# Kernel tuning notes

Hardware: AMD Instinct MI355X
Metric: run time of the kernel (lower is better)

The kernel has to match this reference:

```python
import jax, jax.numpy as jnp
import numpy as np

DIM = 512; H = 8; KH = 2; G = 4; DH = 64        # dim, q heads, kv heads, GQA group, head dim
BALL = 128; SEL = 64; TOPK = 2; PDIM = 3        # sliding ball, compress/selection block, topk, pos dim
SCALE = DH ** -0.5


def _rms_norm(x, gamma):
    return x * jax.lax.rsqrt(jnp.mean(x * x, axis=-1, keepdims=True) + 1e-6) * gamma


def _rotary(t):
    # t: (B, h, S, DH); GPT-NeoX style rotate-half rotary embedding
    S = t.shape[-2]
    inv = 1.0 / (10000.0 ** (jnp.arange(0, DH, 2, dtype=jnp.float32) / DH))
    f = jnp.arange(S, dtype=jnp.float32)[:, None] * inv          # (S, DH/2)
    cos = jnp.concatenate([jnp.cos(f), jnp.cos(f)], -1)
    sin = jnp.concatenate([jnp.sin(f), jnp.sin(f)], -1)
    t1, t2 = jnp.split(t, 2, -1)
    return t * cos + jnp.concatenate([-t2, t1], -1) * sin


def _forward(x, pos, pe_w, pe_b, gamma, wq, wk, wv, k_pos, v_pos,
             k_w1, k_b1, k_w2, k_b2, v_w1, v_b1, v_w2, v_b2,
             mem_k, mem_v, w_combine, w_out, num_batches):
    B = num_batches
    # relative position of leaves wrt ball center (no-grad in original)
    p = jax.lax.stop_gradient(pos).reshape(-1, SEL, PDIM)
    rel = (p - p.mean(axis=1, keepdims=True)).reshape(-1, PDIM)
    x = x + rel @ pe_w + pe_b
    x = x.reshape(B, -1, DIM)
    S = x.shape[1]
    nb = S // SEL
    h = _rms_norm(x, gamma)
    q = (h @ wq).reshape(B, S, H, DH).transpose(0, 2, 1, 3)      # (B,H,S,DH)
    k = (h @ wk).reshape(B, S, KH, DH).transpose(0, 2, 1, 3)     # (B,KH,S,DH)
    v = (h @ wv).reshape(B, S, KH, DH).transpose(0, 2, 1, 3)
    qr, kr = _rotary(q), _rotary(k)

    # --- compressed branch: per-block intra-pos emb + MLP compression ---
    kb = k.reshape(B, KH, nb, SEL, DH) + k_pos[None, :, None]
    vb = v.reshape(B, KH, nb, SEL, DH) + v_pos[None, :, None]
    ck = jax.nn.relu(kb.reshape(B, KH, nb, SEL * DH) @ k_w1 + k_b1) @ k_w2 + k_b2
    cv = jax.nn.relu(vb.reshape(B, KH, nb, SEL * DH) @ v_w1 + v_b1) @ v_w2 + v_b2
    ck = jnp.concatenate([jnp.broadcast_to(mem_k[None], (B, KH, 1, DH)), ck], axis=2)
    cv = jnp.concatenate([jnp.broadcast_to(mem_v[None], (B, KH, 1, DH)), cv], axis=2)
    qg = qr.reshape(B, KH, G, S, DH)
    csim = jnp.einsum('bkgsd,bknd->bkgsn', qg, ck) * SCALE
    cattn = jax.nn.softmax(csim, axis=-1)
    cout = jnp.einsum('bkgsn,bknd->bkgsd', cattn, cv).reshape(B, H, S, DH)

    # --- top-k block selection from compressed attention importance ---
    imp = cattn[..., 1:].mean(axis=2)                            # share over grouped q heads: (B,KH,S,nb)
    imp_blk = imp.reshape(B, KH, nb, SEL, nb).mean(axis=3)       # per query block: (B,KH,nb,nb)
    _, sel = jax.lax.top_k(imp_blk, TOPK)                        # (B,KH,nb,TOPK)

    # --- fine branch: each query block attends own + TOPK selected blocks ---
    kblk = kr.reshape(B, KH, nb, SEL, DH)
    vblk = v.reshape(B, KH, nb, SEL, DH)
    gather = jax.vmap(jax.vmap(lambda t, s: t[s]))               # (nb,SEL,DH),(nb,TOPK)->(nb,TOPK,SEL,DH)
    fk = jnp.concatenate([gather(kblk, sel), kblk[:, :, :, None]], axis=3)
    fv = jnp.concatenate([gather(vblk, sel), vblk[:, :, :, None]], axis=3)
    fk = fk.reshape(B, KH, nb, (TOPK + 1) * SEL, DH)
    fv = fv.reshape(B, KH, nb, (TOPK + 1) * SEL, DH)
    qb = qr.reshape(B, KH, G, nb, SEL, DH)
    fsim = jnp.einsum('bkgnqd,bknmd->bkgnqm', qb, fk) * SCALE
    fout = jnp.einsum('bkgnqm,bknmd->bkgnqd', jax.nn.softmax(fsim, -1), fv)
    fout = fout.reshape(B, H, S, DH)

    # --- sliding branch: MiniBallAttn = plain SDPA within balls of size 128 ---
    nw = S // BALL
    qw = qr.reshape(B, H, nw, BALL, DH)
    kw = jnp.repeat(kr, G, axis=1).reshape(B, H, nw, BALL, DH)
    vw = jnp.repeat(v, G, axis=1).reshape(B, H, nw, BALL, DH)
    ssim = jnp.einsum('bhnqd,bhnkd->bhnqk', qw, kw) * SCALE
    sout = jnp.einsum('bhnqk,bhnkd->bhnqd', jax.nn.softmax(ssim, -1), vw)
    sout = sout.reshape(B, H, S, DH)

    # --- sigmoid-gated strategy combine, merge heads, out projection ---
    gates = jax.nn.sigmoid(h @ w_combine).reshape(B, S, H, 3).transpose(0, 2, 1, 3)
    out = gates[..., 0:1] * cout + gates[..., 1:2] * fout + gates[..., 2:3] * sout
    out = out.transpose(0, 2, 1, 3).reshape(B, S, H * DH) @ w_out
    return out.reshape(-1, DIM)


def setup_inputs() -> dict:
    key = jax.random.key(0)
    ks = jax.random.split(key, 16)
    Bn, S = 8, 4096
    N = Bn * S
    CD = SEL * DH
    def lin(k, fi, fo):
        return (jax.random.normal(k, (fi, fo), jnp.float32) / np.sqrt(fi)).astype(jnp.float32)
    return {
        'x': jax.random.normal(ks[0], (N, DIM), jnp.float32),
        'pos': jax.random.normal(ks[1], (N, PDIM), jnp.float32),
        'pe_w': lin(ks[2], PDIM, DIM),
        'pe_b': jnp.zeros((DIM,), jnp.float32),
        'gamma': jnp.ones((DIM,), jnp.float32),
        'wq': lin(ks[3], DIM, H * DH),
        'wk': lin(ks[4], DIM, KH * DH),
        'wv': lin(ks[5], DIM, KH * DH),
        'k_pos': jax.random.normal(ks[6], (KH, SEL, DH), jnp.float32) * 0.02,
        'v_pos': jax.random.normal(ks[7], (KH, SEL, DH), jnp.float32) * 0.02,
        'k_w1': lin(ks[8], CD, CD), 'k_b1': jnp.zeros((CD,), jnp.float32),
        'k_w2': lin(ks[9], CD, DH), 'k_b2': jnp.zeros((DH,), jnp.float32),
        'v_w1': lin(ks[10], CD, CD), 'v_b1': jnp.zeros((CD,), jnp.float32),
        'v_w2': lin(ks[11], CD, DH), 'v_b2': jnp.zeros((DH,), jnp.float32),
        'mem_k': jax.random.normal(ks[12], (KH, 1, DH), jnp.float32) * 0.02,
        'mem_v': jax.random.normal(ks[13], (KH, 1, DH), jnp.float32) * 0.02,
        'w_combine': lin(ks[14], DIM, 3 * H),
        'w_out': lin(ks[15], H * DH, DIM),
        'num_batches': 8,
    }


def reference(x, pos, pe_w, pe_b, gamma, wq, wk, wv, k_pos, v_pos,
              k_w1, k_b1, k_w2, k_b2, v_w1, v_b1, v_w2, v_b2,
              mem_k, mem_v, w_combine, w_out, num_batches):
    return _forward(x, pos, pe_w, pe_b, gamma, wq, wk, wv, k_pos, v_pos,
                    k_w1, k_b1, k_w2, k_b2, v_w1, v_b1, v_w2, v_b2,
                    mem_k, mem_v, w_combine, w_out, num_batches)
```

## Files before the change

### kernel.cpp

```cpp
#include <hip/hip_runtime.h>
#include <stdint.h>

#define DEVI static __device__ __forceinline__
typedef unsigned short u16;
typedef __bf16 bhalf8 __attribute__((ext_vector_type(8)));
typedef float f32x4 __attribute__((ext_vector_type(4)));

DEVI u16 f2bf(float f) {
  union { float f; unsigned u; } v; v.f = f;
  unsigned r = v.u + 0x7FFFu + ((v.u >> 16) & 1u);
  return (u16)(r >> 16);
}
DEVI float bf2f(u16 h) {
  union { unsigned u; float f; } v; v.u = ((unsigned)h) << 16;
  return v.f;
}
DEVI f32x4 MFMA(bhalf8 a, bhalf8 b, f32x4 c) {
  return __builtin_amdgcn_mfma_f32_16x16x32_bf16(a, b, c, 0, 0, 0);
}
DEVI bhalf8 LD8(const u16* p) { return *(const bhalf8*)p; }
DEVI f32x4 zero4() { f32x4 z = {0.f, 0.f, 0.f, 0.f}; return z; }

#define GLDS16(gp, lp) __builtin_amdgcn_global_load_lds( \
    (const __attribute__((address_space(1))) void*)(gp), \
    (__attribute__((address_space(3))) void*)(lp), 16, 0, 0)


__global__ __launch_bounds__(64) void nsa_pos_mean(const float* __restrict__ pos, float* __restrict__ pm) {
  int blk = blockIdx.x, l = threadIdx.x;
  const float* p = pos + (size_t)(blk * 64 + l) * 3;
  float a = p[0], b = p[1], c = p[2];
#pragma unroll
  for (int o = 32; o; o >>= 1) { a += __shfl_down(a, o); b += __shfl_down(b, o); c += __shfl_down(c, o); }
  if (l == 0) { pm[blk*3+0] = a * (1.f/64.f); pm[blk*3+1] = b * (1.f/64.f); pm[blk*3+2] = c * (1.f/64.f); }
}

__global__ __launch_bounds__(256) void nsa_hnorm(const float* __restrict__ x, const float* __restrict__ pos,
    const float* __restrict__ pm, const float* __restrict__ pew, const float* __restrict__ peb,
    const float* __restrict__ gamma, u16* __restrict__ hhi, u16* __restrict__ hlo) {
  int n = blockIdx.x, t = threadIdx.x;
  int blk = n >> 6;
  float r0 = pos[(size_t)n*3+0] - pm[blk*3+0];
  float r1 = pos[(size_t)n*3+1] - pm[blk*3+1];
  float r2 = pos[(size_t)n*3+2] - pm[blk*3+2];
  int c0 = t, c1 = t + 256;
  const float* xr = x + (size_t)n * 512;
  float v0 = xr[c0] + r0*pew[c0] + r1*pew[512+c0] + r2*pew[1024+c0] + peb[c0];
  float v1 = xr[c1] + r0*pew[c1] + r1*pew[512+c1] + r2*pew[1024+c1] + peb[c1];
  float ss = v0*v0 + v1*v1;
#pragma unroll
  for (int o = 32; o; o >>= 1) ss += __shfl_down(ss, o);
  __shared__ float red[4];
  if ((t & 63) == 0) red[t >> 6] = ss;
  __syncthreads();
  float rms = 1.0f / sqrtf((red[0]+red[1]+red[2]+red[3]) * (1.0f/512.0f) + 1e-6f);
  float h0 = v0 * rms * gamma[c0], h1 = v1 * rms * gamma[c1];
  u16 a0 = f2bf(h0); hhi[(size_t)n*512+c0] = a0; hlo[(size_t)n*512+c0] = f2bf(h0 - bf2f(a0));
  u16 a1 = f2bf(h1); hhi[(size_t)n*512+c1] = a1; hlo[(size_t)n*512+c1] = f2bf(h1 - bf2f(a1));
}

__global__ __launch_bounds__(256) void nsa_wcatT(const float* __restrict__ wq, const float* __restrict__ wk,
    const float* __restrict__ wv, const float* __restrict__ wc, u16* __restrict__ hi, u16* __restrict__ lo) {
  int idx = blockIdx.x * 256 + threadIdx.x;
  if (idx >= 896*512) return;
  int k = idx & 511, n = idx >> 9;
  float v;
  if (n < 512) v = wq[(size_t)k*512 + n];
  else if (n < 640) v = wk[(size_t)k*128 + n - 512];
  else if (n < 768) v = wv[(size_t)k*128 + n - 640];
  else if (n < 792) v = wc[(size_t)k*24 + n - 768];
  else v = 0.f;
  u16 h = f2bf(v); hi[idx] = h; lo[idx] = f2bf(v - bf2f(h));
}

__global__ __launch_bounds__(256) void nsa_rope_tab(float* __restrict__ ct, float* __restrict__ st) {
  int idx = blockIdx.x * 256 + threadIdx.x;
  if (idx >= 4096*32) return;
  int s = idx >> 5, i = idx & 31;
  float e = (float)(2*i) * (1.0f/64.0f);
  float inv = 1.0f / powf(10000.0f, e);
  float f = (float)s * inv;
  ct[idx] = cosf(f); st[idx] = sinf(f);
}

__global__ __launch_bounds__(256) void nsa_rope_k(const float* __restrict__ k32, const float* __restrict__ ct,
    const float* __restrict__ st, u16* __restrict__ kb) {
  int idx = blockIdx.x * 256 + threadIdx.x;
  int d = idx & 31, s = (idx >> 5) & 4095, kh = (idx >> 17) & 1, b = idx >> 18;
  const float* kr = k32 + ((size_t)(b*4096 + s))*128 + kh*64;
  float t1 = kr[d], t2 = kr[d+32];
  float c = ct[s*32+d], sn = st[s*32+d];
  size_t ob = (((size_t)(b*2 + kh))*4096 + s)*64;
  kb[ob+d] = f2bf(t1*c - t2*sn);
  kb[ob+d+32] = f2bf(t2*c + t1*sn);
}

__global__ __launch_bounds__(256) void nsa_vT(const float* __restrict__ v32, u16* __restrict__ vT) {
  int blk = blockIdx.x;
  int st = (blk & 63) * 64, kh = (blk >> 6) & 1, b = blk >> 7;
  __shared__ float tile[64][65];
  int t = threadIdx.x;
  int s = t >> 2, c0 = (t & 3) * 16;
  const float* src = v32 + ((size_t)(b*4096 + st + s))*128 + kh*64;
#pragma unroll
  for (int j = 0; j < 16; ++j) tile[s][c0+j] = src[c0+j];
  __syncthreads();
  int d = t >> 2, s0 = (t & 3) * 16;
  u16* dst = vT + (((size_t)(b*2 + kh))*64 + d)*4096 + st + s0;
#pragma unroll
  for (int j = 0; j < 16; ++j) dst[j] = f2bf(tile[s0+j][d]);
}

__global__ __launch_bounds__(256) void nsa_kb(const float* __restrict__ src, const float* __restrict__ pe,
    u16* __restrict__ ohi, u16* __restrict__ olo) {
  int idx = blockIdx.x * 256 + threadIdx.x;
  int c = idx & 4095, m = idx >> 12;
  int sl = c >> 6, d = c & 63;
  int n = m & 63, kh = (m >> 6) & 1, b = m >> 7;
  int s = n*64 + sl;
  float v = src[((size_t)(b*4096 + s))*128 + kh*64 + d] + pe[(kh*64 + sl)*64 + d];
  u16 h = f2bf(v); ohi[idx] = h;
  if (olo) olo[idx] = f2bf(v - bf2f(h));
}

__global__ __launch_bounds__(256) void nsa_wT(const float* __restrict__ src, u16* __restrict__ dhi,
    u16* __restrict__ dlo, int K, int N) {
  __shared__ float tile[64][65];
  int k0 = blockIdx.x * 64, n0 = blockIdx.y * 64;
  int t = threadIdx.x, r = t >> 2, c0 = (t & 3) * 16;
#pragma unroll
  for (int j = 0; j < 16; ++j) tile[r][c0+j] = src[(size_t)(k0+r)*N + n0 + c0 + j];
  __syncthreads();
  size_t ob = (size_t)(n0 + r)*K + k0 + c0;
#pragma unroll
  for (int j = 0; j < 16; ++j) {
    float v = tile[c0+j][r];
    u16 h = f2bf(v); dhi[ob+j] = h;
    if (dlo) dlo[ob+j] = f2bf(v - bf2f(h));
  }
}

__global__ __launch_bounds__(256) void nsa_init_c(const float* __restrict__ mem, const float* __restrict__ b2,
    float* __restrict__ c32) {
  int idx = blockIdx.x * 256 + threadIdx.x;
  if (idx >= 81920) return;
  int d = idx & 63, n = (idx >> 6) % 80, kh = (idx / (80*64)) & 1;
  c32[idx] = (n == 0) ? mem[kh*64 + d] : ((n <= 64) ? b2[d] : 0.f);
}

__global__ __launch_bounds__(256) void nsa_red64(const float* __restrict__ part, float* __restrict__ c32) {
  int idx = blockIdx.x * 256 + threadIdx.x;
  int m = idx >> 6, d = idx & 63;
  float s = 0.f;
#pragma unroll
  for (int kc = 0; kc < 8; ++kc) s += part[((size_t)kc*1024 + m)*64 + d];
  int bkh = m >> 6, n = m & 63;
  c32[(((size_t)bkh)*80 + 1 + n)*64 + d] += s;
}

template<bool SPLIT>
__global__ __launch_bounds__(256) void nsa_mlp_fuse(const float* __restrict__ part,
    const float* __restrict__ bias, u16* __restrict__ oh, u16* __restrict__ ol) {
  size_t i = ((size_t)blockIdx.x * 256 + threadIdx.x) * 4;
  int c = (int)(i & 4095);
  float4 a = *(const float4*)&part[i];
  float4 b = *(const float4*)&part[(size_t)4194304 + i];
  float v0 = fmaxf(a.x + b.x + bias[c+0], 0.f);
  float v1 = fmaxf(a.y + b.y + bias[c+1], 0.f);
  float v2 = fmaxf(a.z + b.z + bias[c+2], 0.f);
  float v3 = fmaxf(a.w + b.w + bias[c+3], 0.f);
  u16 h0 = f2bf(v0), h1 = f2bf(v1), h2 = f2bf(v2), h3 = f2bf(v3);
  ((unsigned long long*)oh)[i >> 2] = (unsigned long long)h0 | ((unsigned long long)h1 << 16) |
                                      ((unsigned long long)h2 << 32) | ((unsigned long long)h3 << 48);
  if (SPLIT) {
    u16 l0 = f2bf(v0 - bf2f(h0)), l1 = f2bf(v1 - bf2f(h1));
    u16 l2 = f2bf(v2 - bf2f(h2)), l3 = f2bf(v3 - bf2f(h3));
    ((unsigned long long*)ol)[i >> 2] = (unsigned long long)l0 | ((unsigned long long)l1 << 16) |
                                        ((unsigned long long)l2 << 32) | ((unsigned long long)l3 << 48);
  }
}

__global__ __launch_bounds__(256) void nsa_ckcv(const float* __restrict__ ck32, const float* __restrict__ cv32,
    u16* __restrict__ ckh, u16* __restrict__ ckl, u16* __restrict__ cvT) {
  int idx = blockIdx.x * 256 + threadIdx.x;
  if (idx < 81920) {
    float v = ck32[idx];
    u16 h = f2bf(v); ckh[idx] = h; ckl[idx] = f2bf(v - bf2f(h));
  } else if (idx < 81920 + 8*2*64*96) {
    int j = idx - 81920;
    int cc = j % 96, d = (j / 96) & 63, bkh = j / (96*64);
    float v = (cc < 80) ? cv32[((size_t)bkh*80 + cc)*64 + d] : 0.f;
    cvT[j] = f2bf(v);
  }
}

__global__ __launch_bounds__(256) void nsa_comb_bf(const float* __restrict__ c, u16* __restrict__ oh) {
  int i = blockIdx.x * 256 + threadIdx.x;
  float4 v = ((const float4*)c)[i];
  u16 h0 = f2bf(v.x), h1 = f2bf(v.y), h2 = f2bf(v.z), h3 = f2bf(v.w);
  ((unsigned long long*)oh)[i] = (unsigned long long)h0 | ((unsigned long long)h1 << 16) |
                                 ((unsigned long long)h2 << 32) | ((unsigned long long)h3 << 48);
}

__global__ __launch_bounds__(256) void nsa_sentinel(float* __restrict__ o, int n, float val) {
  int i = blockIdx.x * 256 + threadIdx.x;
  if (i < n) o[i] = val;
}

template<bool SPLIT, int EPI>
__global__ __launch_bounds__(256) void nsa_gemm(const u16* __restrict__ Ah, const u16* __restrict__ Al,
    const u16* __restrict__ Bh, const u16* __restrict__ Bl, int K, int N,
    const float* __restrict__ p_cos, float* __restrict__ p_sin,
    u16* __restrict__ out_hi, u16* __restrict__ out_lo,
    float* __restrict__ ok, float* __restrict__ ov, float* __restrict__ og) {
  constexpr int NB = SPLIT ? 4 : 2;
  __shared__ u16 sm[NB * 2 * 4096];
  const int t = threadIdx.x, w = t >> 6, l = t & 63;
  const int wm = w >> 1, wn = w & 1;
  const int MBn = gridDim.x;
  const int nwg = MBn * gridDim.y;
  const int bid = blockIdx.y * MBn + blockIdx.x;
  const int swz = (bid & 7) * (nwg >> 3) + (bid >> 3);
  const int m0 = (swz % MBn) * 128, n0 = (swz / MBn) * 128;
  const int klen = K / (int)gridDim.z;
  const int kb0 = blockIdx.z * klen;
  const int row = l & 15;
  const int kc8 = ((l >> 4) ^ ((l >> 1) & 3)) * 8;
  const int gsc = ((l & 3) ^ ((l >> 3) & 3)) * 8;
  const int sr = l >> 2;
  f32x4 acc[4][4];
#pragma unroll
  for (int a = 0; a < 4; ++a)
#pragma unroll
    for (int b = 0; b < 4; ++b) acc[a][b] = zero4();

  auto STAGE = [&](int buf, int k0) {
    u16* base = sm + buf * NB * 4096;
#pragma unroll
    for (int s2 = 0; s2 < 2; ++s2) {
      int seg = w*2 + s2;
      int r = seg*16 + sr;
      size_t ga = (size_t)(m0 + r)*K + k0 + gsc;
      size_t gb = (size_t)(n0 + r)*K + k0 + gsc;
      GLDS16(&Ah[ga], base + seg*512);
      GLDS16(&Bh[gb], base + 4096 + seg*512);
      if (SPLIT) {
        GLDS16(&Al[ga], base + 2*4096 + seg*512);
        GLDS16(&Bl[gb], base + 3*4096 + seg*512);
      }
    }
  };

  const int nt = klen >> 5;
  STAGE(0, kb0);
  __syncthreads();
  int cur = 0;
  for (int kt = 0; kt < nt; ++kt) {
    if (kt + 1 < nt) STAGE(cur ^ 1, kb0 + (kt + 1) * 32);
    u16* bA  = sm + cur * NB * 4096;
    u16* bB  = bA + 4096;
    u16* bAl = bA + 2*4096;
    u16* bBl = bA + 3*4096;
    bhalf8 af[4], afl[4];
#pragma unroll
    for (int mf = 0; mf < 4; ++mf) {
      af[mf] = LD8(&bA[(wm*64 + mf*16 + row)*32 + kc8]);
      if (SPLIT) afl[mf] = LD8(&bAl[(wm*64 + mf*16 + row)*32 + kc8]);
    }
#pragma unroll
    for (int nf = 0; nf < 4; ++nf) {
      bhalf8 bfh = LD8(&bB[(wn*64 + nf*16 + row)*32 + kc8]);
      bhalf8 bfl;
      if (SPLIT) bfl = LD8(&bBl[(wn*64 + nf*16 + row)*32 + kc8]);
#pragma unroll
      for (int mf = 0; mf < 4; ++mf) {
        acc[mf][nf] = MFMA(af[mf], bfh, acc[mf][nf]);
        if (SPLIT) {
          acc[mf][nf] = MFMA(af[mf], bfl, acc[mf][nf]);
          acc[mf][nf] = MFMA(afl[mf], bfh, acc[mf][nf]);
        }
      }
    }
    __syncthreads();
    cur ^= 1;
  }
  if constexpr (EPI == 0) {
    if (n0 < 512) {
#pragma unroll
      for (int mf = 0; mf < 4; ++mf)
#pragma unroll
        for (int i = 0; i < 4; ++i) {
          int r = m0 + wm*64 + mf*16 + (l >> 4)*4 + i;
          int s = r & 4095, b = r >> 12;
#pragma unroll
          for (int nf = 0; nf < 2; ++nf) {
            int c = n0 + wn*64 + nf*16 + (l & 15);
            int hq = c >> 6, dd = c & 31;
            float t1 = acc[mf][nf][i], t2 = acc[mf][nf+2][i];
            float cs = p_cos[s*32 + dd], sn = p_sin[s*32 + dd];
            float o1 = t1*cs - t2*sn, o2 = t2*cs + t1*sn;
            size_t ob = (((size_t)(b*8 + hq))*4096 + s)*64;
            u16 h1 = f2bf(o1); out_hi[ob+dd] = h1;    out_lo[ob+dd] = f2bf(o1 - bf2f(h1));
            u16 h2 = f2bf(o2); out_hi[ob+dd+32] = h2; out_lo[ob+dd+32] = f2bf(o2 - bf2f(h2));
          }
        }
    } else {
#pragma unroll
      for (int mf = 0; mf < 4; ++mf)
#pragma unroll
        for (int nf = 0; nf < 4; ++nf)
#pragma unroll
          for (int i = 0; i < 4; ++i) {
            int r = m0 + wm*64 + mf*16 + (l >> 4)*4 + i;
            int c = n0 + wn*64 + nf*16 + (l & 15);
            float v = acc[mf][nf][i];
            if (n0 == 512) ok[(size_t)r*128 + (c - 512)] = v;
            else if (n0 == 640) ov[(size_t)r*128 + (c - 640)] = v;
            else if (c < 792) og[(size_t)r*24 + (c - 768)] = 1.0f / (1.0f + expf(-v));
          }
    }
  } else if constexpr (EPI == 2) {
#pragma unroll
    for (int mf = 0; mf < 4; ++mf)
#pragma unroll
      for (int nf = 0; nf < 4; ++nf)
#pragma unroll
        for (int i = 0; i < 4; ++i) {
          int r = m0 + wm*64 + mf*16 + (l >> 4)*4 + i;
          int c = n0 + wn*64 + nf*16 + (l & 15);
          p_sin[(size_t)r*N + c] = acc[mf][nf][i];
        }
  } else {
    const int M = MBn * 128;
#pragma unroll
    for (int mf = 0; mf < 4; ++mf)
#pragma unroll
      for (int nf = 0; nf < 4; ++nf)
#pragma unroll
        for (int i = 0; i < 4; ++i) {
          int r = m0 + wm*64 + mf*16 + (l >> 4)*4 + i;
          int c = n0 + wn*64 + nf*16 + (l & 15);
          p_sin[((size_t)blockIdx.z * M + r) * (size_t)N + c] = acc[mf][nf][i];
        }
  }
}

template<bool SPLIT>
__global__ __launch_bounds__(256) void nsa_gemm64(const u16* __restrict__ Ah, const u16* __restrict__ Al,
    const u16* __restrict__ Bh, const u16* __restrict__ Bl, float* __restrict__ part) {
  constexpr int NB = SPLIT ? 4 : 2;
  __shared__ u16 sm[NB * 2 * 2048];
  const int t = threadIdx.x, w = t >> 6, l = t & 63;
  const int mt = blockIdx.x, kc = blockIdx.y;
  const int row = l & 15;
  const int kc8 = ((l >> 4) ^ ((l >> 1) & 3)) * 8;
  const int gsc = ((l & 3) ^ ((l >> 3) & 3)) * 8;
  const int sr = l >> 2;
  f32x4 acc[4];
#pragma unroll
  for (int a = 0; a < 4; ++a) acc[a] = zero4();

  auto STAGE = [&](int buf, int k0) {
    u16* base = sm + buf * NB * 2048;
    int r = w*16 + sr;
    size_t ga = (size_t)(mt*64 + r)*4096 + k0 + gsc;
    size_t gb = (size_t)r*4096 + k0 + gsc;
    GLDS16(&Ah[ga], base + w*512);
    GLDS16(&Bh[gb], base + 2048 + w*512);
    if (SPLIT) {
      GLDS16(&Al[ga], base + 2*2048 + w*512);
      GLDS16(&Bl[gb], base + 3*2048 + w*512);
    }
  };

  STAGE(0, kc*512);
  __syncthreads();
  int cur = 0;
  for (int kt = 0; kt < 16; ++kt) {
    if (kt + 1 < 16) STAGE(cur ^ 1, kc*512 + (kt + 1) * 32);
    u16* bA  = sm + cur * NB * 2048;
    u16* bB  = bA + 2048;
    u16* bAl = bA + 2*2048;
    u16* bBl = bA + 3*2048;
    bhalf8 a = LD8(&bA[(w*16 + row)*32 + kc8]);
    bhalf8 al;
    if (SPLIT) al = LD8(&bAl[(w*16 + row)*32 + kc8]);
#pragma unroll
    for (int nf = 0; nf < 4; ++nf) {
      bhalf8 b = LD8(&bB[(nf*16 + row)*32 + kc8]);
      bhalf8 bl;
      if (SPLIT) bl = LD8(&bBl[(nf*16 + row)*32 + kc8]);
      acc[nf] = MFMA(a, b, acc[nf]);
      if (SPLIT) {
        acc[nf] = MFMA(a, bl, acc[nf]);
        acc[nf] = MFMA(al, b, acc[nf]);
      }
    }
    __syncthreads();
    cur ^= 1;
  }
#pragma unroll
  for (int nf = 0; nf < 4; ++nf)
#pragma unroll
    for (int i = 0; i < 4; ++i) {
      int m = mt*64 + w*16 + (l >> 4)*4 + i;
      int d = nf*16 + (l & 15);
      part[((size_t)kc*1024 + m)*64 + d] = acc[nf][i];
    }
}


__global__ __launch_bounds__(256) void nsa_attn_comp(const u16* __restrict__ qrh, const u16* __restrict__ qrl,
    const u16* __restrict__ ckh, const u16* __restrict__ ckl, const u16* __restrict__ cvT,
    const float* __restrict__ g32, float* __restrict__ comb, float* __restrict__ imp) {
  __shared__ u16 smem[27392];
  __shared__ float sImp[4 * 80];
  u16* sKh = smem;
  u16* sKl = smem + 5760;
  u16* sVT = smem + 11520;
  u16* sQh = smem + 18176;
  u16* sQl = smem + 22784;
  u16* sP  = smem + 18176;
  const int t = threadIdx.x, w = t >> 6, l = t & 63;
  const int bid = blockIdx.x;
  const int qt = bid & 63, kh = (bid >> 6) & 1, b = bid >> 7;
  const int row = l & 15, kg = (l >> 4) * 8;
  size_t kbase = (size_t)(b*2 + kh) * 80 * 64;
  size_t vbase = (size_t)(b*2 + kh) * 64 * 96;
  for (int e = t; e < 640; e += 256) {
    int r = e >> 3, c = (e & 7) * 8;
    *(int4*)&sKh[r*72 + c] = *(const int4*)&ckh[kbase + r*64 + c];
    *(int4*)&sKl[r*72 + c] = *(const int4*)&ckl[kbase + r*64 + c];
  }
  for (int e = t; e < 768; e += 256) {
    int r = e / 12, ch = e % 12;
    *(int4*)&sVT[r*104 + ch*8] = *(const int4*)&cvT[vbase + (size_t)r*96 + ch*8];
  }
  float accImp = 0.f;
  for (int g = 0; g < 4; ++g) {
    if (g) __syncthreads();
    size_t qbase = ((size_t)((b*2 + kh)*4 + g)*4096 + qt*64) * 64;
    for (int e = t; e < 512; e += 256) {
      int r = e >> 3, c = (e & 7) * 8;
      *(int4*)&sQh[r*72 + c] = *(const int4*)&qrh[qbase + r*64 + c];
      *(int4*)&sQl[r*72 + c] = *(const int4*)&qrl[qbase + r*64 + c];
    }
    __syncthreads();
    f32x4 sc[5];
#pragma unroll
    for (int nf = 0; nf < 5; ++nf) sc[nf] = zero4();
#pragma unroll
    for (int kk = 0; kk < 2; ++kk) {
      bhalf8 ah = LD8(&sQh[(w*16 + row)*72 + kk*32 + kg]);
      bhalf8 al = LD8(&sQl[(w*16 + row)*72 + kk*32 + kg]);
#pragma unroll
      for (int nf = 0; nf < 5; ++nf) {
        bhalf8 bh = LD8(&sKh[(nf*16 + row)*72 + kk*32 + kg]);
        bhalf8 bl = LD8(&sKl[(nf*16 + row)*72 + kk*32 + kg]);
        sc[nf] = MFMA(ah, bh, sc[nf]);
        sc[nf] = MFMA(ah, bl, sc[nf]);
        sc[nf] = MFMA(al, bh, sc[nf]);
      }
    }
    float mx[4] = {-1e30f, -1e30f, -1e30f, -1e30f};
#pragma unroll
    for (int nf = 0; nf < 5; ++nf)
#pragma unroll
      for (int i = 0; i < 4; ++i) {
        int col = nf*16 + (l & 15);
        float v = (col < 65) ? sc[nf][i] * 0.125f : -1e30f;
        sc[nf][i] = v;
        mx[i] = fmaxf(mx[i], v);
      }
#pragma unroll
    for (int i = 0; i < 4; ++i)
#pragma unroll
      for (int o = 1; o < 16; o <<= 1) mx[i] = fmaxf(mx[i], __shfl_xor(mx[i], o));
    float sum[4] = {0.f, 0.f, 0.f, 0.f};
#pragma unroll
    for (int nf = 0; nf < 5; ++nf)
#pragma unroll
      for (int i = 0; i < 4; ++i) {
        int col = nf*16 + (l & 15);
        float p = (col < 65) ? expf(sc[nf][i] - mx[i]) : 0.f;
        sc[nf][i] = p;
        sum[i] += p;
      }
#pragma unroll
    for (int i = 0; i < 4; ++i)
#pragma unroll
      for (int o = 1; o < 16; o <<= 1) sum[i] += __shfl_xor(sum[i], o);
    float inv[4];
#pragma unroll
    for (int i = 0; i < 4; ++i) inv[i] = 1.0f / sum[i];
    __syncthreads();
#pragma unroll
    for (int nf = 0; nf < 5; ++nf)
#pragma unroll
      for (int i = 0; i < 4; ++i)
        sP[(w*16 + (l >> 4)*4 + i)*104 + nf*16 + (l & 15)] = f2bf(sc[nf][i] * inv[i]);
#pragma unroll
    for (int i = 0; i < 4; ++i)
      sP[(w*16 + (l >> 4)*4 + i)*104 + 80 + (l & 15)] = 0;
#pragma unroll
    for (int nf = 0; nf < 5; ++nf) {
      float cs = 0.f;
#pragma unroll
      for (int i = 0; i < 4; ++i) cs += sc[nf][i] * inv[i];
      cs += __shfl_xor(cs, 16);
      cs += __shfl_xor(cs, 32);
      if (l < 16) sImp[w*80 + nf*16 + l] = cs;
    }
    __syncthreads();
    if (t < 64) {
      int n = t + 1;
      accImp += sImp[n] + sImp[80 + n] + sImp[160 + n] + sImp[240 + n];
    }
    f32x4 ov[4];
#pragma unroll
    for (int nf = 0; nf < 4; ++nf) ov[nf] = zero4();
#pragma unroll
    for (int kk = 0; kk < 3; ++kk) {
      bhalf8 a = LD8(&sP[(w*16 + row)*104 + kk*32 + kg]);
#pragma unroll
      for (int nf = 0; nf < 4; ++nf) {
        bhalf8 bv = LD8(&sVT[(nf*16 + row)*104 + kk*32 + kg]);
        ov[nf] = MFMA(a, bv, ov[nf]);
      }
    }
    int hq = kh*4 + g;
#pragma unroll
    for (int i = 0; i < 4; ++i) {
      int q = qt*64 + w*16 + (l >> 4)*4 + i;
      float gate = g32[((size_t)b*4096 + q)*24 + hq*3 + 0];
#pragma unroll
      for (int nf = 0; nf < 4; ++nf) {
        int d = nf*16 + (l & 15);
        comb[(((size_t)b*4096 + q)*8 + hq)*64 + d] = gate * ov[nf][i];
      }
    }
  }
  if (t < 64) imp[(size_t)bid*64 + t] = accImp * (1.0f/256.0f);
}

__global__ __launch_bounds__(64) void nsa_top2(const float* __restrict__ imp, int* __restrict__ sel) {
  int blk = blockIdx.x;
  int l = threadIdx.x;
  float v = imp[(size_t)blk*64 + l];
  float v1 = v; int i1 = l;
#pragma unroll
  for (int o = 1; o < 64; o <<= 1) {
    float ovv = __shfl_xor(v1, o); int oi = __shfl_xor(i1, o);
    if (ovv > v1 || (ovv == v1 && oi < i1)) { v1 = ovv; i1 = oi; }
  }
  float v2 = (l == i1) ? -3.0e38f : v; int i2 = l;
#pragma unroll
  for (int o = 1; o < 64; o <<= 1) {
    float ovv = __shfl_xor(v2, o); int oi = __shfl_xor(i2, o);
    if (ovv > v2 || (ovv == v2 && oi < i2)) { v2 = ovv; i2 = oi; }
  }
  if (l == 0) { sel[blk*2 + 0] = i1; sel[blk*2 + 1] = i2; }
}

__global__ __launch_bounds__(256) void nsa_attn_fine(const u16* __restrict__ qrh, const u16* __restrict__ kr,
    const u16* __restrict__ vT, const int* __restrict__ sel, const float* __restrict__ g32,
    float* __restrict__ comb) {
  __shared__ u16 smem[31232];
  u16* sK  = smem;
  u16* sP  = smem;
  u16* sVT = smem + 13824;
  u16* sQ  = smem + 26624;
  const int t = threadIdx.x, w = t >> 6, l = t & 63;
  const int bid = blockIdx.x;
  const int qt = bid & 63, kh = (bid >> 6) & 1, b = bid >> 7;
  const int row = l & 15, kg = (l >> 4) * 8;
  const int s0 = sel[bid*2 + 0] & 63, s1 = sel[bid*2 + 1] & 63;
  size_t kvb = (size_t)(b*2 + kh) * 4096 * 64;
  size_t vtb = (size_t)(b*2 + kh) * 64 * 4096;
  for (int e = t; e < 1536; e += 256) {
    int r = e / 24, ch = e % 24;
    int n0 = ch * 8, bi = n0 >> 6;
    int blkid = (bi == 0) ? s0 : ((bi == 1) ? s1 : qt);
    int sidx = blkid*64 + (n0 & 63);
    *(int4*)&sVT[r*200 + n0] = *(const int4*)&vT[vtb + (size_t)r*4096 + sidx];
  }
  for (int g = 0; g < 4; ++g) {
    __syncthreads();
    for (int e = t; e < 1536; e += 256) {
      int r = e >> 3, c = (e & 7) * 8;
      int bi = r >> 6;
      int blkid = (bi == 0) ? s0 : ((bi == 1) ? s1 : qt);
      int sidx = blkid*64 + (r & 63);
      *(int4*)&sK[r*72 + c] = *(const int4*)&kr[kvb + (size_t)sidx*64 + c];
    }
    size_t qbase = ((size_t)((b*2 + kh)*4 + g)*4096 + qt*64) * 64;
    for (int e = t; e < 512; e += 256) {
      int r = e >> 3, c = (e & 7) * 8;
      *(int4*)&sQ[r*72 + c] = *(const int4*)&qrh[qbase + r*64 + c];
    }
    __syncthreads();
    f32x4 sc[12];
#pragma unroll
    for (int nf = 0; nf < 12; ++nf) sc[nf] = zero4();
#pragma unroll
    for (int kk = 0; kk < 2; ++kk) {
      bhalf8 a = LD8(&sQ[(w*16 + row)*72 + kk*32 + kg]);
#pragma unroll
      for (int nf = 0; nf < 12; ++nf) {
        bhalf8 bk = LD8(&sK[(nf*16 + row)*72 + kk*32 + kg]);
        sc[nf] = MFMA(a, bk, sc[nf]);
      }
    }
    float mx[4] = {-1e30f, -1e30f, -1e30f, -1e30f};
#pragma unroll
    for (int nf = 0; nf < 12; ++nf)
#pragma unroll
      for (int i = 0; i < 4; ++i) {
        float v = sc[nf][i] * 0.125f;
        sc[nf][i] = v;
        mx[i] = fmaxf(mx[i], v);
      }
#pragma unroll
    for (int i = 0; i < 4; ++i)
#pragma unroll
      for (int o = 1; o < 16; o <<= 1) mx[i] = fmaxf(mx[i], __shfl_xor(mx[i], o));
    float sum[4] = {0.f, 0.f, 0.f, 0.f};
#pragma unroll
    for (int nf = 0; nf < 12; ++nf)
#pragma unroll
      for (int i = 0; i < 4; ++i) {
        float p = expf(sc[nf][i] - mx[i]);
        sc[nf][i] = p;
        sum[i] += p;
      }
#pragma unroll
    for (int i = 0; i < 4; ++i)
#pragma unroll
      for (int o = 1; o < 16; o <<= 1) sum[i] += __shfl_xor(sum[i], o);
    float inv[4];
#pragma unroll
    for (int i = 0; i < 4; ++i) inv[i] = 1.0f / sum[i];
    __syncthreads();
#pragma unroll
    for (int nf = 0; nf < 12; ++nf)
#pragma unroll
      for (int i = 0; i < 4; ++i)
        sP[(w*16 + (l >> 4)*4 + i)*200 + nf*16 + (l & 15)] = f2bf(sc[nf][i] * inv[i]);
    __syncthreads();
    f32x4 ovv[4];
#pragma unroll
    for (int nf = 0; nf < 4; ++nf) ovv[nf] = zero4();
#pragma unroll
    for (int kk = 0; kk < 6; ++kk) {
      bhalf8 a = LD8(&sP[(w*16 + row)*200 + kk*32 + kg]);
#pragma unroll
      for (int nf = 0; nf < 4; ++nf) {
        bhalf8 bv = LD8(&sVT[(nf*16 + row)*200 + kk*32 + kg]);
        ovv[nf] = MFMA(a, bv, ovv[nf]);
      }
    }
    int hq = kh*4 + g;
#pragma unroll
    for (int i = 0; i < 4; ++i) {
      int q = qt*64 + w*16 + (l >> 4)*4 + i;
      float gate = g32[((size_t)b*4096 + q)*24 + hq*3 + 1];
#pragma unroll
      for (int nf = 0; nf < 4; ++nf) {
        int d = nf*16 + (l & 15);
        size_t oi = (((size_t)b*4096 + q)*8 + hq)*64 + d;
        comb[oi] += gate * ovv[nf][i];
      }
    }
  }
}

__global__ __launch_bounds__(256) void nsa_attn_slide(const u16* __restrict__ qrh, const u16* __restrict__ kr,
    const u16* __restrict__ vT, const float* __restrict__ g32, float* __restrict__ comb) {
  __shared__ u16 smem[31232];
  u16* sK  = smem;
  u16* sVT = smem + 9216;
  u16* sQ  = smem + 17920;
  u16* sP  = smem + 22528;
  const int t = threadIdx.x, w = t >> 6, l = t & 63;
  const int bid = blockIdx.x;
  const int ball = bid & 31, kh = (bid >> 5) & 1, b = bid >> 6;
  const int row = l & 15, kg = (l >> 4) * 8;
  const int ks0 = ball * 128;
  size_t kvb = (size_t)(b*2 + kh) * 4096 * 64;
  size_t vtb = (size_t)(b*2 + kh) * 64 * 4096;
  for (int e = t; e < 1024; e += 256) {
    int r = e >> 3, c = (e & 7) * 8;
    *(int4*)&sK[r*72 + c] = *(const int4*)&kr[kvb + (size_t)(ks0 + r)*64 + c];
  }
  for (int e = t; e < 1024; e += 256) {
    int r = e >> 4, ch = e & 15;
    *(int4*)&sVT[r*136 + ch*8] = *(const int4*)&vT[vtb + (size_t)r*4096 + ks0 + ch*8];
  }
  for (int hq = 0; hq < 4; ++hq) {
    int hh = kh*4 + hq;
    for (int qh = 0; qh < 2; ++qh) {
      int qt = ball*2 + qh;
      __syncthreads();
      size_t qbase = ((size_t)(b*8 + hh)*4096 + qt*64) * 64;
      for (int e = t; e < 512; e += 256) {
        int r = e >> 3, c = (e & 7) * 8;
        *(int4*)&sQ[r*72 + c] = *(const int4*)&qrh[qbase + r*64 + c];
      }
      __syncthreads();
      f32x4 sc[8];
#pragma unroll
      for (int nf = 0; nf < 8; ++nf) sc[nf] = zero4();
#pragma unroll
      for (int kk = 0; kk < 2; ++kk) {
        bhalf8 a = LD8(&sQ[(w*16 + row)*72 + kk*32 + kg]);
#pragma unroll
        for (int nf = 0; nf < 8; ++nf) {
          bhalf8 bk = LD8(&sK[(nf*16 + row)*72 + kk*32 + kg]);
          sc[nf] = MFMA(a, bk, sc[nf]);
        }
      }
      float mx[4] = {-1e30f, -1e30f, -1e30f, -1e30f};
#pragma unroll
      for (int nf = 0; nf < 8; ++nf)
#pragma unroll
        for (int i = 0; i < 4; ++i) {
          float v = sc[nf][i] * 0.125f;
          sc[nf][i] = v;
          mx[i] = fmaxf(mx[i], v);
        }
#pragma unroll
      for (int i = 0; i < 4; ++i)
#pragma unroll
        for (int o = 1; o < 16; o <<= 1) mx[i] = fmaxf(mx[i], __shfl_xor(mx[i], o));
      float sum[4] = {0.f, 0.f, 0.f, 0.f};
#pragma unroll
      for (int nf = 0; nf < 8; ++nf)
#pragma unroll
        for (int i = 0; i < 4; ++i) {
          float p = expf(sc[nf][i] - mx[i]);
          sc[nf][i] = p;
          sum[i] += p;
        }
#pragma unroll
      for (int i = 0; i < 4; ++i)
#pragma unroll
        for (int o = 1; o < 16; o <<= 1) sum[i] += __shfl_xor(sum[i], o);
      float inv[4];
#pragma unroll
      for (int i = 0; i < 4; ++i) inv[i] = 1.0f / sum[i];
#pragma unroll
      for (int nf = 0; nf < 8; ++nf)
#pragma unroll
        for (int i = 0; i < 4; ++i)
          sP[(w*16 + (l >> 4)*4 + i)*136 + nf*16 + (l & 15)] = f2bf(sc[nf][i] * inv[i]);
      f32x4 ovv[4];
#pragma unroll
      for (int nf = 0; nf < 4; ++nf) ovv[nf] = zero4();
#pragma unroll
      for (int kk = 0; kk < 4; ++kk) {
        bhalf8 a = LD8(&sP[(w*16 + row)*136 + kk*32 + kg]);
#pragma unroll
        for (int nf = 0; nf < 4; ++nf) {
          bhalf8 bv = LD8(&sVT[(nf*16 + row)*136 + kk*32 + kg]);
          ovv[nf] = MFMA(a, bv, ovv[nf]);
        }
      }
#pragma unroll
      for (int i = 0; i < 4; ++i) {
        int q = qt*64 + w*16 + (l >> 4)*4 + i;
        float gate = g32[((size_t)b*4096 + q)*24 + hh*3 + 2];
#pragma unroll
        for (int nf = 0; nf < 4; ++nf) {
          int d = nf*16 + (l & 15);
          size_t oi = (((size_t)b*4096 + q)*8 + hh)*64 + d;
          comb[oi] += gate * ovv[nf][i];
        }
      }
    }
  }
}


extern "C" void kernel_launch(void* const* d_in, const int* in_sizes, int n_in,
                              void* d_out, int out_size, void* d_ws, size_t ws_size,
                              hipStream_t stream) {
  const float* x     = (const float*)d_in[0];
  const float* pos   = (const float*)d_in[1];
  const float* pe_w  = (const float*)d_in[2];
  const float* pe_b  = (const float*)d_in[3];
  const float* gamma = (const float*)d_in[4];
  const float* wq    = (const float*)d_in[5];
  const float* wk    = (const float*)d_in[6];
  const float* wv    = (const float*)d_in[7];
  const float* k_pos = (const float*)d_in[8];
  const float* v_pos = (const float*)d_in[9];
  const float* k_w1  = (const float*)d_in[10];
  const float* k_b1  = (const float*)d_in[11];
  const float* k_w2  = (const float*)d_in[12];
  const float* k_b2  = (const float*)d_in[13];
  const float* v_w1  = (const float*)d_in[14];
  const float* v_b1  = (const float*)d_in[15];
  const float* v_w2  = (const float*)d_in[16];
  const float* v_b2  = (const float*)d_in[17];
  const float* mem_k = (const float*)d_in[18];
  const float* mem_v = (const float*)d_in[19];
  const float* w_cmb = (const float*)d_in[20];
  const float* w_out = (const float*)d_in[21];
  float* out = (float*)d_out;
  char* ws = (char*)d_ws;

  size_t off = 0;
  auto A = [&](size_t b) { size_t o = off; off += (b + 255) & ~(size_t)255; return o; };
  const size_t oR1 = A(67108864);
  const size_t oR2 = A(67108864);
  const size_t oR4 = A(16777216);
  const size_t oR5 = A(16777216);
  const size_t oR6 = A(16777216);
  const size_t oR7 = A(16777216);
  const size_t oR8 = A(3145728);
  const size_t oR9 = A(2097152);
  const size_t o_cos = A(524288),  o_sin = A(524288);
  const size_t o_pm  = A(8192);
  const size_t o_ck32 = A(327680), o_cv32 = A(327680);
  const size_t o_ckh = A(163840),  o_ckl = A(163840);
  const size_t o_cvT = A(196608);
  const size_t o_woh = A(524288),  o_wol = A(524288);
  const size_t o_imp = A(262144);
  const size_t o_sel = A(8192);
  const size_t o_part = A(2097152);
  const size_t o_part1 = A(33554432);

  if (ws_size < off) {
    nsa_sentinel<<<(out_size + 255)/256, 256, 0, stream>>>(out, out_size, (float)(ws_size >> 20));
    return;
  }

#define WP(T, o) ((T*)(ws + (o)))
  u16*  h_hi = WP(u16, oR1);           u16* h_lo = WP(u16, oR1 + 33554432);
  u16*  w1h  = WP(u16, oR1);           u16* w1l  = WP(u16, oR1 + 33554432);
  float* comb = WP(float, oR1);
  u16*  qrh  = WP(u16, oR2);           u16* qrl  = WP(u16, oR2 + 33554432);
  u16*  cbh  = WP(u16, oR2);
  float* k32 = WP(float, oR4);
  u16*  th   = WP(u16, oR4);           u16* tl   = WP(u16, oR4 + 8388608);
  float* v32 = WP(float, oR5);
  u16*  kbh  = WP(u16, oR6);           u16* kbl  = WP(u16, oR6 + 8388608);
  u16*  krb  = WP(u16, oR7);           u16* vTb  = WP(u16, oR7 + 8388608);
  float* g32 = WP(float, oR8);
  u16*  wch  = WP(u16, oR9);           u16* wcl  = WP(u16, oR9 + 917504);
  u16*  w2h  = WP(u16, oR9);           u16* w2l  = WP(u16, oR9 + 524288);
  u16*  w2vh = WP(u16, oR9 + 1048576); u16* w2vl = WP(u16, oR9 + 1572864);
  float* cosb = WP(float, o_cos);      float* sinb = WP(float, o_sin);
  float* pm  = WP(float, o_pm);
  float* ck32 = WP(float, o_ck32);     float* cv32 = WP(float, o_cv32);
  u16*  ckh  = WP(u16, o_ckh);         u16* ckl  = WP(u16, o_ckl);
  u16*  cvT  = WP(u16, o_cvT);
  u16*  woh  = WP(u16, o_woh);         u16* wol  = WP(u16, o_wol);
  float* imp = WP(float, o_imp);
  int*  selp = WP(int, o_sel);
  float* part = WP(float, o_part);
  float* part1 = WP(float, o_part1);

  nsa_pos_mean<<<512, 64, 0, stream>>>(pos, pm);
  nsa_hnorm<<<32768, 256, 0, stream>>>(x, pos, pm, pe_w, pe_b, gamma, h_hi, h_lo);
  nsa_wcatT<<<1792, 256, 0, stream>>>(wq, wk, wv, w_cmb, wch, wcl);
  nsa_rope_tab<<<512, 256, 0, stream>>>(cosb, sinb);
  nsa_gemm<true, 0><<<dim3(256, 7, 1), 256, 0, stream>>>(h_hi, h_lo, wch, wcl, 512, 896,
      cosb, sinb, qrh, qrl, k32, v32, g32);
  nsa_rope_k<<<8192, 256, 0, stream>>>(k32, cosb, sinb, krb);
  nsa_vT<<<1024, 256, 0, stream>>>(v32, vTb);
  nsa_kb<<<16384, 256, 0, stream>>>(k32, k_pos, kbh, kbl);
  nsa_wT<<<dim3(64, 64), 256, 0, stream>>>(k_w1, w1h, w1l, 4096, 4096);
  nsa_gemm<true, 3><<<dim3(8, 32, 2), 256, 0, stream>>>(kbh, kbl, w1h, w1l, 4096, 4096,
      nullptr, part1, nullptr, nullptr, nullptr, nullptr, nullptr);
  nsa_mlp_fuse<true><<<4096, 256, 0, stream>>>(part1, k_b1, th, tl);
  nsa_wT<<<dim3(64, 1), 256, 0, stream>>>(k_w2, w2h, w2l, 4096, 64);
  nsa_init_c<<<320, 256, 0, stream>>>(mem_k, k_b2, ck32);
  nsa_gemm64<true><<<dim3(16, 8), 256, 0, stream>>>(th, tl, w2h, w2l, part);
  nsa_red64<<<256, 256, 0, stream>>>(part, ck32);
  nsa_kb<<<16384, 256, 0, stream>>>(v32, v_pos, kbh, nullptr);
  nsa_wT<<<dim3(64, 64), 256, 0, stream>>>(v_w1, w1h, nullptr, 4096, 4096);
  nsa_gemm<false, 3><<<dim3(8, 32, 2), 256, 0, stream>>>(kbh, nullptr, w1h, nullptr, 4096, 4096,
      nullptr, part1, nullptr, nullptr, nullptr, nullptr, nullptr);
  nsa_mlp_fuse<false><<<4096, 256, 0, stream>>>(part1, v_b1, th, nullptr);
  nsa_wT<<<dim3(64, 1), 256, 0, stream>>>(v_w2, w2vh, nullptr, 4096, 64);
  nsa_init_c<<<320, 256, 0, stream>>>(mem_v, v_b2, cv32);
  nsa_gemm64<false><<<dim3(16, 8), 256, 0, stream>>>(th, nullptr, w2vh, nullptr, part);
  nsa_red64<<<256, 256, 0, stream>>>(part, cv32);
  nsa_ckcv<<<704, 256, 0, stream>>>(ck32, cv32, ckh, ckl, cvT);
  nsa_attn_comp<<<1024, 256, 0, stream>>>(qrh, qrl, ckh, ckl, cvT, g32, comb, imp);
  nsa_top2<<<1024, 64, 0, stream>>>(imp, selp);
  nsa_attn_fine<<<1024, 256, 0, stream>>>(qrh, krb, vTb, selp, g32, comb);
  nsa_attn_slide<<<512, 256, 0, stream>>>(qrh, krb, vTb, g32, comb);
  nsa_comb_bf<<<16384, 256, 0, stream>>>(comb, cbh);
  nsa_wT<<<dim3(8, 8), 256, 0, stream>>>(w_out, woh, nullptr, 512, 512);
  nsa_gemm<false, 2><<<dim3(256, 4, 1), 256, 0, stream>>>(cbh, nullptr, woh, nullptr, 512, 512,
      nullptr, out, nullptr, nullptr, nullptr, nullptr, nullptr);
#undef WP
}
```

Baseline: 737.9 us.

## Fuse K/V post-processing into QKV GEMM epilogue and bf16 cast into slide attention

The QKV GEMM epilogue now applies rotary to K, builds the k_pos-added hi/lo block inputs for the compression MLP, and writes V as bf16 plus the v_pos-added block input directly. This removes the fp32 K/V round trips and the separate rope_k, kb and comb_bf kernels. The V transpose now works from bf16 instead of fp32, and the sliding-window attention writes the final bf16 combined output itself. The QKV GEMM also gets a custom XCD-aware tile mapping. In exchange the GEMM epilogue does more scattered stores, and the V path is rounded to bf16 before the transpose.

```diff
diff --git a/kernel.cpp b/kernel.cpp
--- a/kernel.cpp
+++ b/kernel.cpp
@@ -83,44 +83,20 @@
   ct[idx] = cosf(f); st[idx] = sinf(f);
 }
 
-__global__ __launch_bounds__(256) void nsa_rope_k(const float* __restrict__ k32, const float* __restrict__ ct,
-    const float* __restrict__ st, u16* __restrict__ kb) {
-  int idx = blockIdx.x * 256 + threadIdx.x;
-  int d = idx & 31, s = (idx >> 5) & 4095, kh = (idx >> 17) & 1, b = idx >> 18;
-  const float* kr = k32 + ((size_t)(b*4096 + s))*128 + kh*64;
-  float t1 = kr[d], t2 = kr[d+32];
-  float c = ct[s*32+d], sn = st[s*32+d];
-  size_t ob = (((size_t)(b*2 + kh))*4096 + s)*64;
-  kb[ob+d] = f2bf(t1*c - t2*sn);
-  kb[ob+d+32] = f2bf(t2*c + t1*sn);
-}
-
-__global__ __launch_bounds__(256) void nsa_vT(const float* __restrict__ v32, u16* __restrict__ vT) {
+__global__ __launch_bounds__(256) void nsa_vT16(const u16* __restrict__ v16, u16* __restrict__ vT) {
   int blk = blockIdx.x;
-  int st = (blk & 63) * 64, kh = (blk >> 6) & 1, b = blk >> 7;
-  __shared__ float tile[64][65];
+  int st = (blk & 63) * 64, bkh = blk >> 6;
+  __shared__ u16 tile[64][72];
   int t = threadIdx.x;
   int s = t >> 2, c0 = (t & 3) * 16;
-  const float* src = v32 + ((size_t)(b*4096 + st + s))*128 + kh*64;
-#pragma unroll
-  for (int j = 0; j < 16; ++j) tile[s][c0+j] = src[c0+j];
+  const u16* src = v16 + ((size_t)bkh*4096 + st + s) * 64;
+  *(int4*)&tile[s][c0]   = *(const int4*)&src[c0];
+  *(int4*)&tile[s][c0+8] = *(const int4*)&src[c0+8];
   __syncthreads();
   int d = t >> 2, s0 = (t & 3) * 16;
-  u16* dst = vT + (((size_t)(b*2 + kh))*64 + d)*4096 + st + s0;
-#pragma unroll
-  for (int j = 0; j < 16; ++j) dst[j] = f2bf(tile[s0+j][d]);
-}
-
-__global__ __launch_bounds__(256) void nsa_kb(const float* __restrict__ src, const float* __restrict__ pe,
-    u16* __restrict__ ohi, u16* __restrict__ olo) {
-  int idx = blockIdx.x * 256 + threadIdx.x;
-  int c = idx & 4095, m = idx >> 12;
-  int sl = c >> 6, d = c & 63;
-  int n = m & 63, kh = (m >> 6) & 1, b = m >> 7;
-  int s = n*64 + sl;
-  float v = src[((size_t)(b*4096 + s))*128 + kh*64 + d] + pe[(kh*64 + sl)*64 + d];
-  u16 h = f2bf(v); ohi[idx] = h;
-  if (olo) olo[idx] = f2bf(v - bf2f(h));
+  u16* dst = vT + ((size_t)bkh*64 + d)*4096 + st + s0;
+#pragma unroll
+  for (int j = 0; j < 16; ++j) dst[j] = tile[s0+j][d];
 }
 
 __global__ __launch_bounds__(256) void nsa_wT(const float* __restrict__ src, u16* __restrict__ dhi,
@@ -194,14 +170,6 @@
   }
 }
 
-__global__ __launch_bounds__(256) void nsa_comb_bf(const float* __restrict__ c, u16* __restrict__ oh) {
-  int i = blockIdx.x * 256 + threadIdx.x;
-  float4 v = ((const float4*)c)[i];
-  u16 h0 = f2bf(v.x), h1 = f2bf(v.y), h2 = f2bf(v.z), h3 = f2bf(v.w);
-  ((unsigned long long*)oh)[i] = (unsigned long long)h0 | ((unsigned long long)h1 << 16) |
-                                 ((unsigned long long)h2 << 32) | ((unsigned long long)h3 << 48);
-}
-
 __global__ __launch_bounds__(256) void nsa_sentinel(float* __restrict__ o, int n, float val) {
   int i = blockIdx.x * 256 + threadIdx.x;
   if (i < n) o[i] = val;
@@ -211,17 +179,29 @@
 __global__ __launch_bounds__(256) void nsa_gemm(const u16* __restrict__ Ah, const u16* __restrict__ Al,
     const u16* __restrict__ Bh, const u16* __restrict__ Bl, int K, int N,
     const float* __restrict__ p_cos, float* __restrict__ p_sin,
-    u16* __restrict__ out_hi, u16* __restrict__ out_lo,
-    float* __restrict__ ok, float* __restrict__ ov, float* __restrict__ og) {
+    u16* __restrict__ out_hi, u16* __restrict__ out_lo, float* __restrict__ og,
+    const float* __restrict__ kpos, const float* __restrict__ vpos,
+    u16* __restrict__ krb, u16* __restrict__ kbh, u16* __restrict__ kbl,
+    u16* __restrict__ v16o, u16* __restrict__ vbh) {
   constexpr int NB = SPLIT ? 4 : 2;
   __shared__ u16 sm[NB * 2 * 4096];
   const int t = threadIdx.x, w = t >> 6, l = t & 63;
   const int wm = w >> 1, wn = w & 1;
-  const int MBn = gridDim.x;
-  const int nwg = MBn * gridDim.y;
-  const int bid = blockIdx.y * MBn + blockIdx.x;
-  const int swz = (bid & 7) * (nwg >> 3) + (bid >> 3);
-  const int m0 = (swz % MBn) * 128, n0 = (swz / MBn) * 128;
+  int m0, n0;
+  if constexpr (EPI == 0) {
+    const int bid = blockIdx.y * 256 + blockIdx.x;
+    const int xcd = bid & 7, j = bid >> 3;
+    const int mg = j / 56, rem = j % 56;
+    const int nn = rem >> 3, mi = rem & 7;
+    m0 = ((xcd * 4 + mg) * 8 + mi) * 128;
+    n0 = nn * 128;
+  } else {
+    const int MBn = gridDim.x;
+    const int nwg = MBn * gridDim.y;
+    const int bid = blockIdx.y * MBn + blockIdx.x;
+    const int swz = (bid & 7) * (nwg >> 3) + (bid >> 3);
+    m0 = (swz % MBn) * 128; n0 = (swz / MBn) * 128;
+  }
   const int klen = K / (int)gridDim.z;
   const int kb0 = blockIdx.z * klen;
   const int row = l & 15;
@@ -304,6 +284,53 @@
             u16 h2 = f2bf(o2); out_hi[ob+dd+32] = h2; out_lo[ob+dd+32] = f2bf(o2 - bf2f(h2));
           }
         }
+    } else if (n0 == 512) {
+      int kh = wn;
+#pragma unroll
+      for (int mf = 0; mf < 4; ++mf)
+#pragma unroll
+        for (int i = 0; i < 4; ++i) {
+          int r = m0 + wm*64 + mf*16 + (l >> 4)*4 + i;
+          int s = r & 4095, b = r >> 12;
+          int n = s >> 6, sl = s & 63;
+          size_t krbase = ((size_t)(b*2 + kh)*4096 + s)*64;
+          size_t kbbase = ((size_t)(b*128 + kh*64 + n))*4096 + sl*64;
+#pragma unroll
+          for (int nf = 0; nf < 2; ++nf) {
+            int dd = nf*16 + (l & 15);
+            float t1 = acc[mf][nf][i], t2 = acc[mf][nf+2][i];
+            float cs = p_cos[s*32 + dd], sn = p_sin[s*32 + dd];
+            krb[krbase + dd]      = f2bf(t1*cs - t2*sn);
+            krb[krbase + dd + 32] = f2bf(t2*cs + t1*sn);
+          }
+#pragma unroll
+          for (int nf = 0; nf < 4; ++nf) {
+            int dk = nf*16 + (l & 15);
+            float v = acc[mf][nf][i] + kpos[(kh*64 + sl)*64 + dk];
+            u16 h = f2bf(v);
+            kbh[kbbase + dk] = h;
+            kbl[kbbase + dk] = f2bf(v - bf2f(h));
+          }
+        }
+    } else if (n0 == 640) {
+      int kh = wn;
+#pragma unroll
+      for (int mf = 0; mf < 4; ++mf)
+#pragma unroll
+        for (int i = 0; i < 4; ++i) {
+          int r = m0 + wm*64 + mf*16 + (l >> 4)*4 + i;
+          int s = r & 4095, b = r >> 12;
+          int n = s >> 6, sl = s & 63;
+          size_t v16base = ((size_t)(b*2 + kh)*4096 + s)*64;
+          size_t vbbase = ((size_t)(b*128 + kh*64 + n))*4096 + sl*64;
+#pragma unroll
+          for (int nf = 0; nf < 4; ++nf) {
+            int dv = nf*16 + (l & 15);
+            float vv = acc[mf][nf][i];
+            v16o[v16base + dv] = f2bf(vv);
+            vbh[vbbase + dv] = f2bf(vv + vpos[(kh*64 + sl)*64 + dv]);
+          }
+        }
     } else {
 #pragma unroll
       for (int mf = 0; mf < 4; ++mf)
@@ -313,10 +340,7 @@
           for (int i = 0; i < 4; ++i) {
             int r = m0 + wm*64 + mf*16 + (l >> 4)*4 + i;
             int c = n0 + wn*64 + nf*16 + (l & 15);
-            float v = acc[mf][nf][i];
-            if (n0 == 512) ok[(size_t)r*128 + (c - 512)] = v;
-            else if (n0 == 640) ov[(size_t)r*128 + (c - 640)] = v;
-            else if (c < 792) og[(size_t)r*24 + (c - 768)] = 1.0f / (1.0f + expf(-v));
+            if (c < 792) og[(size_t)r*24 + (c - 768)] = 1.0f / (1.0f + expf(-acc[mf][nf][i]));
           }
     }
   } else if constexpr (EPI == 2) {
@@ -331,7 +355,7 @@
           p_sin[(size_t)r*N + c] = acc[mf][nf][i];
         }
   } else {
-    const int M = MBn * 128;
+    const int M = (int)gridDim.x * 128;
 #pragma unroll
     for (int mf = 0; mf < 4; ++mf)
 #pragma unroll
@@ -675,7 +699,8 @@
 }
 
 __global__ __launch_bounds__(256) void nsa_attn_slide(const u16* __restrict__ qrh, const u16* __restrict__ kr,
-    const u16* __restrict__ vT, const float* __restrict__ g32, float* __restrict__ comb) {
+    const u16* __restrict__ vT, const float* __restrict__ g32, const float* __restrict__ comb,
+    u16* __restrict__ cbh) {
   __shared__ u16 smem[31232];
   u16* sK  = smem;
   u16* sVT = smem + 9216;
@@ -773,7 +798,7 @@
         for (int nf = 0; nf < 4; ++nf) {
           int d = nf*16 + (l & 15);
           size_t oi = (((size_t)b*4096 + q)*8 + hh)*64 + d;
-          comb[oi] += gate * ovv[nf][i];
+          cbh[oi] = f2bf(comb[oi] + gate * ovv[nf][i]);
         }
       }
     }
@@ -840,10 +865,8 @@
   u16*  w1h  = WP(u16, oR1);           u16* w1l  = WP(u16, oR1 + 33554432);
   float* comb = WP(float, oR1);
   u16*  qrh  = WP(u16, oR2);           u16* qrl  = WP(u16, oR2 + 33554432);
-  u16*  cbh  = WP(u16, oR2);
-  float* k32 = WP(float, oR4);
   u16*  th   = WP(u16, oR4);           u16* tl   = WP(u16, oR4 + 8388608);
-  float* v32 = WP(float, oR5);
+  u16*  v16b = WP(u16, oR5);           u16* vbh  = WP(u16, oR5 + 8388608);
   u16*  kbh  = WP(u16, oR6);           u16* kbl  = WP(u16, oR6 + 8388608);
   u16*  krb  = WP(u16, oR7);           u16* vTb  = WP(u16, oR7 + 8388608);
   float* g32 = WP(float, oR8);
@@ -860,28 +883,28 @@
   int*  selp = WP(int, o_sel);
   float* part = WP(float, o_part);
   float* part1 = WP(float, o_part1);
+  u16*  cbh  = WP(u16, o_part1);
 
   nsa_pos_mean<<<512, 64, 0, stream>>>(pos, pm);
   nsa_hnorm<<<32768, 256, 0, stream>>>(x, pos, pm, pe_w, pe_b, gamma, h_hi, h_lo);
   nsa_wcatT<<<1792, 256, 0, stream>>>(wq, wk, wv, w_cmb, wch, wcl);
   nsa_rope_tab<<<512, 256, 0, stream>>>(cosb, sinb);
   nsa_gemm<true, 0><<<dim3(256, 7, 1), 256, 0, stream>>>(h_hi, h_lo, wch, wcl, 512, 896,
-      cosb, sinb, qrh, qrl, k32, v32, g32);
-  nsa_rope_k<<<8192, 256, 0, stream>>>(k32, cosb, sinb, krb);
-  nsa_vT<<<1024, 256, 0, stream>>>(v32, vTb);
-  nsa_kb<<<16384, 256, 0, stream>>>(k32, k_pos, kbh, kbl);
+      cosb, sinb, qrh, qrl, g32, k_pos, v_pos, krb, kbh, kbl, v16b, vbh);
+  nsa_vT16<<<1024, 256, 0, stream>>>(v16b, vTb);
   nsa_wT<<<dim3(64, 64), 256, 0, stream>>>(k_w1, w1h, w1l, 4096, 4096);
   nsa_gemm<true, 3><<<dim3(8, 32, 2), 256, 0, stream>>>(kbh, kbl, w1h, w1l, 4096, 4096,
-      nullptr, part1, nullptr, nullptr, nullptr, nullptr, nullptr);
+      nullptr, part1, nullptr, nullptr, nullptr, nullptr, nullptr, nullptr, nullptr, nullptr,
+      nullptr, nullptr);
   nsa_mlp_fuse<true><<<4096, 256, 0, stream>>>(part1, k_b1, th, tl);
   nsa_wT<<<dim3(64, 1), 256, 0, stream>>>(k_w2, w2h, w2l, 4096, 64);
   nsa_init_c<<<320, 256, 0, stream>>>(mem_k, k_b2, ck32);
   nsa_gemm64<true><<<dim3(16, 8), 256, 0, stream>>>(th, tl, w2h, w2l, part);
   nsa_red64<<<256, 256, 0, stream>>>(part, ck32);
-  nsa_kb<<<16384, 256, 0, stream>>>(v32, v_pos, kbh, nullptr);
   nsa_wT<<<dim3(64, 64), 256, 0, stream>>>(v_w1, w1h, nullptr, 4096, 4096);
-  nsa_gemm<false, 3><<<dim3(8, 32, 2), 256, 0, stream>>>(kbh, nullptr, w1h, nullptr, 4096, 4096,
-      nullptr, part1, nullptr, nullptr, nullptr, nullptr, nullptr);
+  nsa_gemm<false, 3><<<dim3(8, 32, 2), 256, 0, stream>>>(vbh, nullptr, w1h, nullptr, 4096, 4096,
+      nullptr, part1, nullptr, nullptr, nullptr, nullptr, nullptr, nullptr, nullptr, nullptr,
+      nullptr, nullptr);
   nsa_mlp_fuse<false><<<4096, 256, 0, stream>>>(part1, v_b1, th, nullptr);
   nsa_wT<<<dim3(64, 1), 256, 0, stream>>>(v_w2, w2vh, nullptr, 4096, 64);
   nsa_init_c<<<320, 256, 0, stream>>>(mem_v, v_b2, cv32);
@@ -891,10 +914,10 @@
   nsa_attn_comp<<<1024, 256, 0, stream>>>(qrh, qrl, ckh, ckl, cvT, g32, comb, imp);
   nsa_top2<<<1024, 64, 0, stream>>>(imp, selp);
   nsa_attn_fine<<<1024, 256, 0, stream>>>(qrh, krb, vTb, selp, g32, comb);
-  nsa_attn_slide<<<512, 256, 0, stream>>>(qrh, krb, vTb, g32, comb);
-  nsa_comb_bf<<<16384, 256, 0, stream>>>(comb, cbh);
+  nsa_attn_slide<<<512, 256, 0, stream>>>(qrh, krb, vTb, g32, comb, cbh);
   nsa_wT<<<dim3(8, 8), 256, 0, stream>>>(w_out, woh, nullptr, 512, 512);
   nsa_gemm<false, 2><<<dim3(256, 4, 1), 256, 0, stream>>>(cbh, nullptr, woh, nullptr, 512, 512,
-      nullptr, out, nullptr, nullptr, nullptr, nullptr, nullptr);
+      nullptr, out, nullptr, nullptr, nullptr, nullptr, nullptr, nullptr, nullptr, nullptr,
+      nullptr, nullptr);
 #undef WP
 }
```

Result: faster. 697.7 us (-5.4%).
